# Performance work log

Measured on AMD Instinct MI355X. Metric: run time of the kernel, lower is better.

The kernel has to match this reference:

```python
import jax, jax.numpy as jnp
import numpy as np

D = 768; H = 12; DH = 64; P = 16; G = 14; NP = 196; L = 197
LD = 4; GD = 12          # local / latent depths
RL = 12; RG = 8          # tokens merged per layer (total_merge // depth)
B = 8
EPS = 1e-6


def layernorm(x, g, b):
    mu = x.mean(-1, keepdims=True)
    v = ((x - mu) ** 2).mean(-1, keepdims=True)
    return (x - mu) / jnp.sqrt(v + EPS) * g + b


def attention(x, size, qkv_w, qkv_b, pw, pb):
    # proportional attention: logits += log(token size)
    Bn, N, _ = x.shape
    qkv = (x @ qkv_w + qkv_b).reshape(Bn, N, 3, H, DH)
    q, k, v = (qkv[:, :, i].transpose(0, 2, 1, 3) for i in range(3))  # bhnd
    logits = jnp.einsum('bhqd,bhkd->bhqk', q, k) * (DH ** -0.5)
    logits = logits + jnp.log(size)[:, None, None, :, 0]
    a = jax.nn.softmax(logits, axis=-1)
    o = jnp.einsum('bhqk,bhkd->bhqd', a, v).transpose(0, 2, 1, 3).reshape(Bn, N, D)
    return o @ pw + pb, k.mean(1)  # metric = mean key over heads


def tome_merge(x, size, metric, r, tok_map):
    # ToMe bipartite soft matching + weighted-average merge + source-map update
    Bn, N, _ = x.shape
    t1, t2 = (N + 1) // 2, N // 2
    m = metric / jnp.linalg.norm(metric, axis=-1, keepdims=True)
    scores = jnp.einsum('bid,bjd->bij', m[:, ::2], m[:, 1::2])
    scores = scores.at[:, 0, :].set(-jnp.inf)  # protect cls token
    node_max, node_idx = scores.max(-1), scores.argmax(-1).astype(jnp.int32)
    order = jnp.argsort(-node_max, axis=-1).astype(jnp.int32)
    src_idx = order[:, :r]
    unm_idx = jnp.sort(order[:, r:], axis=-1)  # cls stays first
    dst_idx = jnp.take_along_axis(node_idx, src_idx, axis=1)
    bi = jnp.arange(Bn)[:, None]

    def merge_sum(v):
        a, b = v[:, ::2], v[:, 1::2]
        unm = jnp.take_along_axis(a, unm_idx[..., None], axis=1)
        s = jnp.take_along_axis(a, src_idx[..., None], axis=1)
        b = b.at[bi, dst_idx].add(s)
        return jnp.concatenate([unm, b], axis=1)

    new_size = merge_sum(size)
    new_x = merge_sum(x * size) / new_size
    # per-step old->new index map, then compose with running source map
    pos_a = jnp.zeros((Bn, t1), jnp.int32)
    pos_a = pos_a.at[bi, unm_idx].set(jnp.arange(t1 - r, dtype=jnp.int32))
    pos_a = pos_a.at[bi, src_idx].set((t1 - r) + dst_idx)
    step = jnp.zeros((Bn, N), jnp.int32)
    step = step.at[:, ::2].set(pos_a)
    step = step.at[:, 1::2].set((t1 - r) + jnp.arange(t2, dtype=jnp.int32)[None])
    return new_x, new_size, jnp.take_along_axis(step, tok_map, axis=1)


def encode(x, size, tok_map, r, p):
    ln1g, ln1b, qw, qb, pw, pb, ln2g, ln2b, f1w, f1b, f2w, f2b = p
    for i in range(ln1g.shape[0]):
        a, metric = attention(layernorm(x, ln1g[i], ln1b[i]), size, qw[i], qb[i], pw[i], pb[i])
        x = x + a
        if r > 0:
            x, size, tok_map = tome_merge(x, size, metric, r, tok_map)
        h = layernorm(x, ln2g[i], ln2b[i])
        x = x + (jax.nn.gelu(h @ f1w[i] + f1b[i], approximate=False) @ f2w[i] + f2b[i])
    return x, size, tok_map


def setup_inputs() -> dict:
    key = jax.random.key(0)
    ks = iter(jax.random.split(key, 64))
    def w(shape):
        return jax.random.normal(next(ks), shape, jnp.float32) * 0.02
    def blocks(d, pre):
        return {pre + 'ln1g': jnp.ones((d, D)), pre + 'ln1b': jnp.zeros((d, D)),
                pre + 'qkv_w': w((d, D, 3 * D)), pre + 'qkv_b': jnp.zeros((d, 3 * D)),
                pre + 'proj_w': w((d, D, D)), pre + 'proj_b': jnp.zeros((d, D)),
                pre + 'ln2g': jnp.ones((d, D)), pre + 'ln2b': jnp.zeros((d, D)),
                pre + 'fc1w': w((d, D, 4 * D)), pre + 'fc1b': jnp.zeros((d, 4 * D)),
                pre + 'fc2w': w((d, 4 * D, D)), pre + 'fc2b': jnp.zeros((d, D))}
    inp = dict(x=jax.random.normal(next(ks), (B, 3, 224, 224), jnp.float32),
               patch_w=w((3 * P * P, D)), patch_b=jnp.zeros((D,)),
               cls_tok=w((1, 1, D)), pos_emb=w((1, L, D)),
               l_ng=jnp.ones((D,)), l_nb=jnp.zeros((D,)),
               g_ng=jnp.ones((D,)), g_nb=jnp.zeros((D,)),
               head_w=w((D, 10)), head_b=jnp.zeros((10,)))
    inp.update(blocks(LD, 'l_'))
    inp.update(blocks(GD, 'g_'))
    return inp


def reference(x, patch_w, patch_b, cls_tok, pos_emb,
              l_ln1g, l_ln1b, l_qkv_w, l_qkv_b, l_proj_w, l_proj_b,
              l_ln2g, l_ln2b, l_fc1w, l_fc1b, l_fc2w, l_fc2b, l_ng, l_nb,
              g_ln1g, g_ln1b, g_qkv_w, g_qkv_b, g_proj_w, g_proj_b,
              g_ln2g, g_ln2b, g_fc1w, g_fc1b, g_fc2w, g_fc2b, g_ng, g_nb,
              head_w, head_b):
    Bn = x.shape[0]
    # non-overlapping 16x16 patchify == conv stride 16
    patches = x.reshape(Bn, 3, G, P, G, P).transpose(0, 2, 4, 1, 3, 5).reshape(Bn, NP, 3 * P * P)
    t = patches @ patch_w + patch_b
    t = jnp.concatenate([jnp.broadcast_to(cls_tok, (Bn, 1, D)), t], axis=1) + pos_emb
    size = jnp.ones((Bn, L, 1), t.dtype)
    tmap = jnp.broadcast_to(jnp.arange(L, dtype=jnp.int32)[None], (Bn, L))  # token_map_for_dtem
    lp = (l_ln1g, l_ln1b, l_qkv_w, l_qkv_b, l_proj_w, l_proj_b, l_ln2g, l_ln2b, l_fc1w, l_fc1b, l_fc2w, l_fc2b)
    xl, size, tmap = encode(t, size, tmap, RL, lp)   # local encoder: 197 -> 149 tokens
    xl = layernorm(xl, l_ng, l_nb)
    N1 = xl.shape[1]
    smap = jnp.broadcast_to(jnp.arange(N1, dtype=jnp.int32)[None], (Bn, N1))  # latent source_map
    gp = (g_ln1g, g_ln1b, g_qkv_w, g_qkv_b, g_proj_w, g_proj_b, g_ln2g, g_ln2b, g_fc1w, g_fc1b, g_fc2w, g_fc2b)
    xg, size, smap = encode(xl, size, smap, RG, gp)  # latent encoder: 149 -> 53 tokens
    xg = layernorm(xg, g_ng, g_nb)
    xr = jnp.take_along_axis(xg, smap[..., None], axis=1)   # token_unmerge_from_map (ToMe)
    xf = jnp.take_along_axis(xr, tmap[..., None], axis=1)   # token_unmerge_from_map_for_dtem
    return xf[:, 0] @ head_w + head_b  # cls token -> logits (B, 10)
```

## Files before the change

### kernel.cpp

```cpp
#include <hip/hip_runtime.h>
#include <math.h>

#define NB 8
#define SD 768
#define NHEAD 12
#define LMAX 197
#define QBLK 32
#define KBLK 64

typedef __attribute__((ext_vector_type(8))) short bf16x8;
typedef __attribute__((ext_vector_type(4))) float f32x4;
typedef const __attribute__((address_space(1))) unsigned int gu32_t;
typedef __attribute__((address_space(3))) unsigned int lu32_t;

static __device__ __forceinline__ float geluf(float x){
    return 0.5f*x*(1.0f+erff(x*0.70710678118654752440f));
}

static __device__ __forceinline__ void split_bf16(float v, ushort& h, ushort& l){
    uint u = __float_as_uint(v);
    uint hb = (u + 0x7FFFu + ((u>>16)&1u)) >> 16;
    h = (ushort)hb;
    float rem = v - __uint_as_float(hb<<16);
    uint u2 = __float_as_uint(rem);
    l = (ushort)((u2 + 0x7FFFu + ((u2>>16)&1u)) >> 16);
}

__global__ __launch_bounds__(256) void wconv(const float* __restrict__ W,
        ushort* __restrict__ Hi, ushort* __restrict__ Lo, int K, int Nc)
{
    __shared__ float tile[32][33];
    int z = blockIdx.z;
    const float* Wz = W + (size_t)z*K*Nc;
    ushort* Hz = Hi + (size_t)z*Nc*K;
    ushort* Lz = Lo + (size_t)z*Nc*K;
    int n0 = blockIdx.x*32, k0 = blockIdx.y*32;
    int tx = threadIdx.x&31, ty = threadIdx.x>>5;
    #pragma unroll
    for (int i=0;i<32;i+=8) tile[ty+i][tx] = Wz[(size_t)(k0+ty+i)*Nc + n0+tx];
    __syncthreads();
    #pragma unroll
    for (int i=0;i<32;i+=8){
        float v = tile[tx][ty+i];
        ushort h,l; split_bf16(v,h,l);
        size_t o = (size_t)(n0+ty+i)*K + k0+tx;
        Hz[o]=h; Lz[o]=l;
    }
}

template<int EPI, int SPLITK>
__global__ __launch_bounds__(256) void gemm_mfma(const ushort* __restrict__ AHi,
        const ushort* __restrict__ ALo, const ushort* __restrict__ WHi,
        const ushort* __restrict__ WLo, const float* __restrict__ bias,
        const float* __restrict__ R, float* __restrict__ C,
        ushort* __restrict__ CHi, ushort* __restrict__ CLo,
        float* __restrict__ Part, int M, int Nc, int K, int ntok, int gx)
{
    __shared__ __align__(16) ushort sAhi[2][2048], sAlo[2][2048];
    __shared__ __align__(16) ushort sBhi[2][2048], sBlo[2][2048];
    const int t = threadIdx.x;
    const int nwg = gridDim.x;
    const int qc = nwg>>3, rc = nwg&7;
    const int xcd = blockIdx.x & 7, jj = blockIdx.x >> 3;
    const int wid = (xcd<rc ? xcd*(qc+1) : rc*(qc+1)+(xcd-rc)*qc) + jj;
    const int bx = wid % gx;
    const int t2 = wid / gx;
    const int gy = nwg/(gx*SPLITK);
    const int by = t2 % gy;
    const int bz = t2 / gy;

    const int w = t>>6, l = t&63, lr = l&15, lg = l>>4;
    const int wr = w>>1, wc = w&1;

    const int Ks = K/SPLITK;
    const int kbeg = bz*Ks;
    const int nt = Ks/32;

    const int srow = t>>2;
    const uint schunk = (uint)((((t&3) ^ ((t>>3)&3)))*16);
    int ar = by*64 + srow; if (ar >= M) ar = M-1;
    int ab_ = ar/ntok; int an_ = ar - ab_*ntok;
    size_t aoff = ((size_t)(ab_*LMAX+an_)*K + kbeg)*2 + schunk;
    size_t woff = ((size_t)(bx*64+srow)*K + kbeg)*2 + schunk;
    const char* pAh = (const char*)AHi + aoff;
    const char* pAl = (const char*)ALo + aoff;
    const char* pWh = (const char*)WHi + woff;
    const char* pWl = (const char*)WLo + woff;

    f32x4 acc[2][2];
    #pragma unroll
    for (int i=0;i<2;i++)
        #pragma unroll
        for (int j=0;j<2;j++) acc[i][j] = (f32x4){0.f,0.f,0.f,0.f};

    const uint wb = (uint)(w*512);

    auto stage = [&](int bf, int kt){
        size_t ko = (size_t)kt*64;
        __builtin_amdgcn_global_load_lds((gu32_t*)(pAh+ko), (lu32_t*)&sAhi[bf][wb], 16, 0, 0);
        __builtin_amdgcn_global_load_lds((gu32_t*)(pAl+ko), (lu32_t*)&sAlo[bf][wb], 16, 0, 0);
        __builtin_amdgcn_global_load_lds((gu32_t*)(pWh+ko), (lu32_t*)&sBhi[bf][wb], 16, 0, 0);
        __builtin_amdgcn_global_load_lds((gu32_t*)(pWl+ko), (lu32_t*)&sBlo[bf][wb], 16, 0, 0);
    };

    int buf = 0;
    stage(0, 0);
    for (int kt=0; kt<nt; ++kt){
        if (kt+1 < nt){
            stage(buf^1, kt+1);
            asm volatile("s_waitcnt vmcnt(4)" ::: "memory");
        } else {
            asm volatile("s_waitcnt vmcnt(0)" ::: "memory");
        }
        __builtin_amdgcn_s_barrier();
        bf16x8 ah[2], al[2], bh[2], bl[2];
        #pragma unroll
        for (int m=0;m<2;m++){
            int row = wr*32 + m*16 + lr;
            uint off = (uint)(row*64 + ((lg ^ ((row>>1)&3))<<4));
            ah[m] = *(const bf16x8*)((const char*)&sAhi[buf][0] + off);
            al[m] = *(const bf16x8*)((const char*)&sAlo[buf][0] + off);
        }
        #pragma unroll
        for (int n=0;n<2;n++){
            int col = wc*32 + n*16 + lr;
            uint off = (uint)(col*64 + ((lg ^ ((col>>1)&3))<<4));
            bh[n] = *(const bf16x8*)((const char*)&sBhi[buf][0] + off);
            bl[n] = *(const bf16x8*)((const char*)&sBlo[buf][0] + off);
        }
        #pragma unroll
        for (int m=0;m<2;m++)
            #pragma unroll
            for (int n=0;n<2;n++){
                acc[m][n] = __builtin_amdgcn_mfma_f32_16x16x32_bf16(ah[m], bh[n], acc[m][n], 0,0,0);
                acc[m][n] = __builtin_amdgcn_mfma_f32_16x16x32_bf16(ah[m], bl[n], acc[m][n], 0,0,0);
                acc[m][n] = __builtin_amdgcn_mfma_f32_16x16x32_bf16(al[m], bh[n], acc[m][n], 0,0,0);
            }
        __builtin_amdgcn_s_barrier();
        buf ^= 1;
    }

    if (SPLITK > 1){
        float* Pz = Part + (size_t)bz*M*Nc;
        #pragma unroll
        for (int m=0;m<2;m++){
            #pragma unroll
            for (int n=0;n<2;n++){
                int gcol = bx*64 + wc*32 + n*16 + lr;
                #pragma unroll
                for (int r=0;r<4;r++){
                    int grow = by*64 + wr*32 + m*16 + lg*4 + r;
                    if (grow >= M) continue;
                    Pz[(size_t)grow*Nc + gcol] = acc[m][n][r];
                }
            }
        }
    } else {
        #pragma unroll
        for (int m=0;m<2;m++){
            #pragma unroll
            for (int n=0;n<2;n++){
                int gcol = bx*64 + wc*32 + n*16 + lr;
                float bv = bias[gcol];
                #pragma unroll
                for (int r=0;r<4;r++){
                    int grow = by*64 + wr*32 + m*16 + lg*4 + r;
                    if (grow >= M) continue;
                    int b = grow/ntok; int ni = grow - b*ntok;
                    size_t off = (size_t)(b*LMAX+ni)*Nc + gcol;
                    float v = acc[m][n][r] + bv;
                    if (EPI==1){
                        v = geluf(v);
                        ushort h,lo; split_bf16(v,h,lo);
                        CHi[off]=h; CLo[off]=lo;
                    } else {
                        if (EPI==2) v += R[off];
                        C[off] = v;
                    }
                }
            }
        }
    }
}

__global__ __launch_bounds__(256) void reduce_k(const float* __restrict__ P,
        const float* __restrict__ bias, const float* __restrict__ R,
        float* __restrict__ C, int M, int Nc, int S, int ntok)
{
    int idx = blockIdx.x*256 + threadIdx.x;
    int tot = M*(Nc/4);
    if (idx >= tot) return;
    int grow = idx/(Nc/4), c4 = idx - grow*(Nc/4);
    size_t po = (size_t)grow*Nc + c4*4;
    float4 a = *(const float4*)(P + po);
    for (int s=1;s<S;s++){
        float4 v = *(const float4*)(P + (size_t)s*M*Nc + po);
        a.x+=v.x; a.y+=v.y; a.z+=v.z; a.w+=v.w;
    }
    int b = grow/ntok, n = grow - b*ntok;
    size_t off = (size_t)(b*LMAX+n)*Nc + c4*4;
    float4 bv = *(const float4*)(bias + c4*4);
    float4 rv = *(const float4*)(R + off);
    float4 o;
    o.x=a.x+bv.x+rv.x; o.y=a.y+bv.y+rv.y; o.z=a.z+bv.z+rv.z; o.w=a.w+bv.w+rv.w;
    *(float4*)(C + off) = o;
}

__device__ __forceinline__ float block_sum256(float v){
    __shared__ float red[4];
    for (int o=32;o>0;o>>=1) v += __shfl_down(v,o,64);
    int t=threadIdx.x;
    if ((t&63)==0) red[t>>6]=v;
    __syncthreads();
    float r = red[0]+red[1]+red[2]+red[3];
    __syncthreads();
    return r;
}

__global__ __launch_bounds__(256) void ln_split(const float* __restrict__ X,
        const float* __restrict__ gam, const float* __restrict__ bet,
        ushort* __restrict__ YHi, ushort* __restrict__ YLo)
{
    int n = blockIdx.x, b = blockIdx.y, t = threadIdx.x;
    const float* xr = X + ((size_t)(b*LMAX+n))*SD;
    size_t ro = ((size_t)(b*LMAX+n))*SD;
    float v0=xr[t], v1=xr[t+256], v2=xr[t+512];
    float mu = block_sum256(v0+v1+v2) * (1.0f/768.0f);
    float d0=v0-mu, d1=v1-mu, d2=v2-mu;
    float var = block_sum256(d0*d0+d1*d1+d2*d2) * (1.0f/768.0f);
    float rs = rsqrtf(var + 1e-6f);
    float y0 = d0*rs*gam[t]     + bet[t];
    float y1 = d1*rs*gam[t+256] + bet[t+256];
    float y2 = d2*rs*gam[t+512] + bet[t+512];
    ushort h,lo;
    split_bf16(y0,h,lo); YHi[ro+t]=h;     YLo[ro+t]=lo;
    split_bf16(y1,h,lo); YHi[ro+t+256]=h; YLo[ro+t+256]=lo;
    split_bf16(y2,h,lo); YHi[ro+t+512]=h; YLo[ro+t+512]=lo;
}

__global__ __launch_bounds__(256) void ln_kernel(const float* __restrict__ X,
        const float* __restrict__ gam, const float* __restrict__ bet,
        float* __restrict__ Y)
{
    int n = blockIdx.x, b = blockIdx.y, t = threadIdx.x;
    const float* xr = X + ((size_t)(b*LMAX+n))*SD;
    float* yr = Y + ((size_t)(b*LMAX+n))*SD;
    float v0=xr[t], v1=xr[t+256], v2=xr[t+512];
    float mu = block_sum256(v0+v1+v2) * (1.0f/768.0f);
    float d0=v0-mu, d1=v1-mu, d2=v2-mu;
    float var = block_sum256(d0*d0+d1*d1+d2*d2) * (1.0f/768.0f);
    float rs = rsqrtf(var + 1e-6f);
    yr[t]     = d0*rs*gam[t]     + bet[t];
    yr[t+256] = d1*rs*gam[t+256] + bet[t+256];
    yr[t+512] = d2*rs*gam[t+512] + bet[t+512];
}

__global__ __launch_bounds__(256) void attn_tile(const float* __restrict__ QKV,
        const float* __restrict__ SZ, ushort* __restrict__ OHi,
        ushort* __restrict__ OLo, int N)
{
    const int q0 = blockIdx.x*QBLK;
    const int h = blockIdx.y, b = blockIdx.z, t = threadIdx.x;
    __shared__ float Qs[QBLK][68];
    __shared__ float KVs[KBLK][68];
    __shared__ float Ls[QBLK][200];
    __shared__ float szl[KBLK];
    __shared__ float invs[QBLK];

    {
        int row = t>>3, seg = t&7;
        int q = q0 + row;
        if (q < N){
            const float* src = QKV + ((size_t)(b*LMAX+q))*2304 + h*64 + seg*8;
            *(float4*)&Qs[row][seg*8]   = *(const float4*)src;
            *(float4*)&Qs[row][seg*8+4] = *(const float4*)(src+4);
        } else {
            float4 z = make_float4(0.f,0.f,0.f,0.f);
            *(float4*)&Qs[row][seg*8]   = z;
            *(float4*)&Qs[row][seg*8+4] = z;
        }
    }
    const int tq = t>>3, tk = t&7;
    const int nkt = (N+KBLK-1)/KBLK;

    for (int kt=0; kt<nkt; ++kt){
        int kbase = kt*KBLK;
        __syncthreads();
        {
            int row = t>>2, seg = t&3;
            int ktok = kbase + row;
            float4 a,b4,c,d4;
            if (ktok < N){
                const float* src = QKV + ((size_t)(b*LMAX+ktok))*2304 + 768 + h*64 + seg*16;
                a=*(const float4*)src; b4=*(const float4*)(src+4);
                c=*(const float4*)(src+8); d4=*(const float4*)(src+12);
            } else {
                a=b4=c=d4=make_float4(0.f,0.f,0.f,0.f);
            }
            *(float4*)&KVs[row][seg*16]   =a;
            *(float4*)&KVs[row][seg*16+4] =b4;
            *(float4*)&KVs[row][seg*16+8] =c;
            *(float4*)&KVs[row][seg*16+12]=d4;
            if (t < KBLK){
                int kk2 = kbase + t;
                szl[t] = (kk2<N) ? logf(SZ[b*LMAX+kk2]) : 0.f;
            }
        }
        __syncthreads();
        float acc[8];
        #pragma unroll
        for (int j=0;j<8;j++) acc[j]=0.f;
        #pragma unroll 4
        for (int d4=0; d4<16; ++d4){
            float4 qv = *(const float4*)&Qs[tq][d4*4];
            #pragma unroll
            for (int j=0;j<8;j++){
                float4 kv = *(const float4*)&KVs[tk+8*j][d4*4];
                acc[j] += qv.x*kv.x + qv.y*kv.y + qv.z*kv.z + qv.w*kv.w;
            }
        }
        #pragma unroll
        for (int j=0;j<8;j++){
            int kk = kbase + tk + 8*j;
            if (kk < N) Ls[tq][kk] = acc[j]*0.125f + szl[tk+8*j];
        }
    }
    __syncthreads();

    {
        float m = -INFINITY;
        for (int k=tk;k<N;k+=8) m = fmaxf(m, Ls[tq][k]);
        #pragma unroll
        for (int o=1;o<8;o<<=1) m = fmaxf(m, __shfl_xor(m,o,64));
        float s = 0.f;
        for (int k=tk;k<N;k+=8){
            float p = expf(Ls[tq][k]-m);
            Ls[tq][k]=p; s+=p;
        }
        #pragma unroll
        for (int o=1;o<8;o<<=1) s += __shfl_xor(s,o,64);
        if (tk==0) invs[tq] = 1.0f/s;
    }

    float o0[8];
    #pragma unroll
    for (int i=0;i<8;i++) o0[i]=0.f;
    for (int kt=0; kt<nkt; ++kt){
        int kbase = kt*KBLK;
        __syncthreads();
        {
            int row = t>>2, seg = t&3;
            int ktok = kbase + row;
            float4 a,b4,c,d4;
            if (ktok < N){
                const float* src = QKV + ((size_t)(b*LMAX+ktok))*2304 + 1536 + h*64 + seg*16;
                a=*(const float4*)src; b4=*(const float4*)(src+4);
                c=*(const float4*)(src+8); d4=*(const float4*)(src+12);
            } else {
                a=b4=c=d4=make_float4(0.f,0.f,0.f,0.f);
            }
            *(float4*)&KVs[row][seg*16]   =a;
            *(float4*)&KVs[row][seg*16+4] =b4;
            *(float4*)&KVs[row][seg*16+8] =c;
            *(float4*)&KVs[row][seg*16+12]=d4;
        }
        __syncthreads();
        int kmax = N - kbase; if (kmax > KBLK) kmax = KBLK;
        for (int kk=0; kk<kmax; ++kk){
            float p = Ls[tq][kbase+kk];
            float4 v0 = *(const float4*)&KVs[kk][tk*8];
            float4 v1 = *(const float4*)&KVs[kk][tk*8+4];
            o0[0]+=p*v0.x; o0[1]+=p*v0.y; o0[2]+=p*v0.z; o0[3]+=p*v0.w;
            o0[4]+=p*v1.x; o0[5]+=p*v1.y; o0[6]+=p*v1.z; o0[7]+=p*v1.w;
        }
    }
    int q = q0 + tq;
    if (q < N){
        float inv = invs[tq];
        ushort hh[8], ll[8];
        #pragma unroll
        for (int i=0;i<8;i++){ split_bf16(o0[i]*inv, hh[i], ll[i]); }
        size_t o = ((size_t)(b*LMAX+q))*SD + h*64 + tk*8;
        *(ushort4*)(OHi+o)   = make_ushort4(hh[0],hh[1],hh[2],hh[3]);
        *(ushort4*)(OHi+o+4) = make_ushort4(hh[4],hh[5],hh[6],hh[7]);
        *(ushort4*)(OLo+o)   = make_ushort4(ll[0],ll[1],ll[2],ll[3]);
        *(ushort4*)(OLo+o+4) = make_ushort4(ll[4],ll[5],ll[6],ll[7]);
    }
}

__global__ void metric_k(const float* __restrict__ QKV, float* __restrict__ MET)
{
    const int n = blockIdx.x, b = blockIdx.y, d = threadIdx.x;
    const float* base = QKV + ((size_t)(b*LMAX+n))*2304 + 768 + d;
    float s=0.f;
    #pragma unroll
    for (int h=0;h<12;h++) s += base[h*64];
    s *= (1.0f/12.0f);
    float sq = s*s;
    for (int o=32;o>0;o>>=1) sq += __shfl_down(sq,o,64);
    float nrm = sqrtf(__shfl(sq,0,64));
    MET[((size_t)(b*LMAX+n))*64 + d] = s/nrm;
}

__global__ __launch_bounds__(128) void scores_k(const float* __restrict__ MET,
        float* __restrict__ NMAX, int* __restrict__ NIDX, int t2)
{
    const int i = blockIdx.x, b = blockIdx.y, t = threadIdx.x;
    __shared__ float ma[64];
    __shared__ float vals[128];
    __shared__ int idxs[128];
    if (t<64) ma[t] = MET[((size_t)(b*LMAX+2*i))*64+t];
    __syncthreads();
    float val = -INFINITY;
    if (t<t2 && i>0){
        const float* mb = MET + ((size_t)(b*LMAX+2*t+1))*64;
        float dot=0.f;
        #pragma unroll 8
        for (int dd=0;dd<64;dd++) dot += ma[dd]*mb[dd];
        val = dot;
    }
    vals[t]=val; idxs[t]=t; __syncthreads();
    for (int s=64;s>0;s>>=1){
        if (t<s){
            float v2=vals[t+s], v1=vals[t]; int i2=idxs[t+s];
            if (v2>v1 || (v2==v1 && i2<idxs[t])){ vals[t]=v2; idxs[t]=i2; }
        }
        __syncthreads();
    }
    if (t==0){ NMAX[b*128+i]=vals[0]; NIDX[b*128+i]=idxs[0]; }
}

__global__ __launch_bounds__(128) void plan_k(const float* __restrict__ NMAX,
        const int* __restrict__ NIDX, int* __restrict__ SRC, int* __restrict__ DST,
        int* __restrict__ STEP, int* __restrict__ INV, int t1, int t2, int r)
{
    const int b = blockIdx.x, i = threadIdx.x;
    __shared__ float nm[128];
    __shared__ int issrc[128];
    nm[i] = (i<t1) ? NMAX[b*128+i] : INFINITY;
    __syncthreads();
    int rank=0, is=0, ni=0;
    if (i<t1){
        float m = nm[i];
        for (int j=0;j<t1;j++){ float a=nm[j]; if (a>m || (a==m && j<i)) rank++; }
        is = (rank<r) ? 1:0;
        ni = NIDX[b*128+i];
    }
    issrc[i]=is; __syncthreads();
    if (i<t1){
        if (is){ SRC[b*16+rank]=i; DST[b*16+rank]=ni; STEP[b*LMAX+2*i] = t1-r+ni; }
        else {
            int cnt=0;
            for (int j=0;j<i;j++) cnt += 1-issrc[j];
            STEP[b*LMAX+2*i]=cnt;
            INV[b*LMAX+cnt]=2*i;
        }
    }
    if (i<t2){ STEP[b*LMAX+2*i+1]=t1-r+i; INV[b*LMAX+(t1-r)+i]=2*i+1; }
}

__global__ __launch_bounds__(256) void merge_fused(const float* __restrict__ X,
        const float* __restrict__ SZ, const int* __restrict__ INV,
        const int* __restrict__ SRC, const int* __restrict__ DST,
        float* __restrict__ XO, float* __restrict__ SZO, int t1, int r)
{
    int p = blockIdx.x, b = blockIdx.y, t = threadIdx.x;
    int base = t1 - r;
    float acc0, acc1, acc2, snew;
    if (p < base){
        int tok = INV[b*LMAX+p];
        float s = SZ[b*LMAX+tok];
        const float* xr = X + (size_t)(b*LMAX+tok)*SD;
        acc0=xr[t]*s; acc1=xr[t+256]*s; acc2=xr[t+512]*s; snew=s;
    } else {
        int d = p - base;
        int tok = 2*d+1;
        float s = SZ[b*LMAX+tok];
        const float* xr = X + (size_t)(b*LMAX+tok)*SD;
        acc0=xr[t]*s; acc1=xr[t+256]*s; acc2=xr[t+512]*s; snew=s;
        for (int k=0;k<r;k++){
            if (DST[b*16+k]==d){
                int st = 2*SRC[b*16+k];
                float ss = SZ[b*LMAX+st];
                const float* xs = X + (size_t)(b*LMAX+st)*SD;
                acc0+=xs[t]*ss; acc1+=xs[t+256]*ss; acc2+=xs[t+512]*ss; snew+=ss;
            }
        }
    }
    float inv = 1.0f/snew;
    float* o = XO + (size_t)(b*LMAX+p)*SD;
    o[t]=acc0*inv; o[t+256]=acc1*inv; o[t+512]=acc2*inv;
    if (t==0) SZO[b*LMAX+p]=snew;
}

__global__ void map_upd(int* __restrict__ MAP, const int* __restrict__ STEP, int mlen)
{
    int i = blockIdx.x*256+threadIdx.x;
    if (i >= NB*mlen) return;
    int b=i/mlen, t=i-b*mlen;
    MAP[b*LMAX+t] = STEP[b*LMAX + MAP[b*LMAX+t]];
}

__global__ void patchify(const float* __restrict__ X, ushort* __restrict__ PHi,
        ushort* __restrict__ PLo)
{
    size_t i = (size_t)blockIdx.x*256 + threadIdx.x;
    if (i >= (size_t)NB*196*768) return;
    int f = i % 768; size_t q = i/768; int p = q % 196; int b = q/196;
    int c = f >> 8, py = (f>>4)&15, px = f&15;
    int gy = p/14, gx = p - gy*14;
    float v = X[(((size_t)b*3 + c)*224 + gy*16+py)*224 + gx*16+px];
    ushort h,l; split_bf16(v,h,l);
    size_t o = ((size_t)(b*LMAX+p))*768 + f;
    PHi[o]=h; PLo[o]=l;
}

__global__ void assemble(const float* __restrict__ T, const float* __restrict__ cls,
        const float* __restrict__ pos, float* __restrict__ Xo)
{
    size_t i = (size_t)blockIdx.x*256 + threadIdx.x;
    if (i >= (size_t)NB*LMAX*768) return;
    int d = i % 768; size_t q = i/768; int n = q % LMAX; int b = q/LMAX;
    float v = (n==0) ? cls[d] : T[((size_t)(b*LMAX+n-1))*768+d];
    Xo[((size_t)(b*LMAX+n))*768+d] = v + pos[n*768+d];
}

__global__ void init_state(float* __restrict__ SZ, int* __restrict__ TMAP, int* __restrict__ SMAP)
{
    int i = blockIdx.x*256+threadIdx.x;
    if (i >= NB*LMAX) return;
    SZ[i]=1.0f;
    int n=i%LMAX;
    TMAP[i]=n;
    if (n<149) SMAP[i]=n;
}

__global__ void head_k(const float* __restrict__ XG, const int* __restrict__ SMAP,
        const int* __restrict__ TMAP, const float* __restrict__ HW,
        const float* __restrict__ HB, float* __restrict__ OUT)
{
    int t = threadIdx.x;
    if (t>=80) return;
    int b=t/10, o=t-b*10;
    int row = SMAP[b*LMAX + TMAP[b*LMAX]];
    const float* xr = XG + ((size_t)(b*LMAX+row))*SD;
    float acc = HB[o];
    for (int d=0;d<SD;d++) acc += xr[d]*HW[d*10+o];
    OUT[b*10+o]=acc;
}

extern "C" void kernel_launch(void* const* d_in, const int* in_sizes, int n_in,
                              void* d_out, int out_size, void* d_ws, size_t ws_size,
                              hipStream_t stream)
{
    const float* x_in    = (const float*)d_in[0];
    const float* patch_w = (const float*)d_in[1];
    const float* patch_b = (const float*)d_in[2];
    const float* cls     = (const float*)d_in[3];
    const float* pos     = (const float*)d_in[4];
    const float* l_ng    = (const float*)d_in[5];
    const float* l_nb    = (const float*)d_in[6];
    const float* g_ng    = (const float*)d_in[7];
    const float* g_nb    = (const float*)d_in[8];
    const float* head_w  = (const float*)d_in[9];
    const float* head_b  = (const float*)d_in[10];
    const float* L[12];  for (int i=0;i<12;i++) L[i]  = (const float*)d_in[11+i];
    const float* Gp[12]; for (int i=0;i<12;i++) Gp[i] = (const float*)d_in[23+i];
    float* out = (float*)d_out;

    float* fp = (float*)d_ws;
    float* xA      = fp; fp += (size_t)NB*LMAX*SD;
    float* xB      = fp; fp += (size_t)NB*LMAX*SD;
    float* qkvbuf  = fp; fp += (size_t)NB*LMAX*2304;
    float* metricbuf=fp; fp += (size_t)NB*LMAX*64;
    float* partbuf = fp; fp += (size_t)4*NB*LMAX*SD;
    float* szA     = fp; fp += NB*LMAX;
    float* szB     = fp; fp += NB*LMAX;
    float* nodemax = fp; fp += NB*128;
    int* ip = (int*)fp;
    int* tmap    = ip; ip += NB*LMAX;
    int* smap    = ip; ip += NB*LMAX;
    int* stepbuf = ip; ip += NB*LMAX;
    int* invrow  = ip; ip += NB*LMAX;
    int* nodeidx = ip; ip += NB*128;
    int* srcs    = ip; ip += NB*16;
    int* dsts    = ip; ip += NB*16;
    uintptr_t up = ((uintptr_t)ip + 15) & ~(uintptr_t)15;
    ushort* sp = (ushort*)up;
    ushort* lnHi = sp; sp += (size_t)NB*LMAX*SD;
    ushort* lnLo = sp; sp += (size_t)NB*LMAX*SD;
    ushort* oHi  = sp; sp += (size_t)NB*LMAX*SD;
    ushort* oLo  = sp; sp += (size_t)NB*LMAX*SD;
    ushort* hHi  = sp; sp += (size_t)NB*LMAX*3072;
    ushort* hLo  = sp; sp += (size_t)NB*LMAX*3072;
    ushort* pHi  = sp; sp += (size_t)NB*LMAX*SD;
    ushort* pLo  = sp; sp += (size_t)NB*LMAX*SD;
    ushort* patchHi = sp; sp += (size_t)768*768;
    ushort* patchLo = sp; sp += (size_t)768*768;
    ushort* qkvHi = sp; sp += (size_t)4*768*2304;
    ushort* qkvLo = sp; sp += (size_t)4*768*2304;
    ushort* projHi= sp; sp += (size_t)4*768*768;
    ushort* projLo= sp; sp += (size_t)4*768*768;
    ushort* fc1Hi = sp; sp += (size_t)4*768*3072;
    ushort* fc1Lo = sp; sp += (size_t)4*768*3072;
    ushort* fc2Hi = sp; sp += (size_t)4*3072*768;
    ushort* fc2Lo = sp; sp += (size_t)4*3072*768;

    float *xc = xA, *xn = xB, *szc = szA, *szn = szB;

    auto conv_chunk = [&](const float* qw, const float* pw, const float* f1w,
                          const float* f2w, int nz)
    {
        wconv<<<dim3(2304/32,768/32,nz),256,0,stream>>>(qw, qkvHi, qkvLo, SD, 2304);
        wconv<<<dim3(768/32,768/32,nz),256,0,stream>>>(pw, projHi, projLo, SD, SD);
        wconv<<<dim3(3072/32,768/32,nz),256,0,stream>>>(f1w, fc1Hi, fc1Lo, SD, 3072);
        wconv<<<dim3(768/32,3072/32,nz),256,0,stream>>>(f2w, fc2Hi, fc2Lo, 3072, SD);
    };

    auto run_block = [&](const float* ln1g, const float* ln1b, const float* qb,
                         const float* pb, const float* ln2g, const float* ln2b,
                         const float* f1b, const float* f2b,
                         int slot, int N, int r, int* mp, int mlen)
    {
        int M = NB*N;
        int Mt = (M+63)/64;
        const ushort* qH = qkvHi + (size_t)slot*768*2304;
        const ushort* qL = qkvLo + (size_t)slot*768*2304;
        const ushort* pH = projHi + (size_t)slot*768*768;
        const ushort* pL = projLo + (size_t)slot*768*768;
        const ushort* f1H = fc1Hi + (size_t)slot*768*3072;
        const ushort* f1L = fc1Lo + (size_t)slot*768*3072;
        const ushort* f2H = fc2Hi + (size_t)slot*3072*768;
        const ushort* f2L = fc2Lo + (size_t)slot*3072*768;

        ln_split<<<dim3(N,NB),256,0,stream>>>(xc, ln1g, ln1b, lnHi, lnLo);
        gemm_mfma<0,1><<<36*Mt,256,0,stream>>>(lnHi, lnLo, qH, qL, qb, nullptr, qkvbuf, nullptr, nullptr, nullptr, M, 2304, SD, N, 36);
        attn_tile<<<dim3((N+QBLK-1)/QBLK,NHEAD,NB),256,0,stream>>>(qkvbuf, szc, oHi, oLo, N);
        metric_k<<<dim3(N,NB),64,0,stream>>>(qkvbuf, metricbuf);
        gemm_mfma<0,4><<<12*Mt*4,256,0,stream>>>(oHi, oLo, pH, pL, nullptr, nullptr, nullptr, nullptr, nullptr, partbuf, M, SD, SD, N, 12);
        reduce_k<<<(M*(SD/4)+255)/256,256,0,stream>>>(partbuf, pb, xc, xc, M, SD, 4, N);
        int t1=(N+1)/2, t2=N/2, Nn=N-r;
        scores_k<<<dim3(t1,NB),128,0,stream>>>(metricbuf, nodemax, nodeidx, t2);
        plan_k<<<NB,128,0,stream>>>(nodemax, nodeidx, srcs, dsts, stepbuf, invrow, t1, t2, r);
        merge_fused<<<dim3(Nn,NB),256,0,stream>>>(xc, szc, invrow, srcs, dsts, xn, szn, t1, r);
        map_upd<<<(NB*mlen+255)/256,256,0,stream>>>(mp, stepbuf, mlen);
        int M2 = NB*Nn;
        int M2t = (M2+63)/64;
        ln_split<<<dim3(Nn,NB),256,0,stream>>>(xn, ln2g, ln2b, lnHi, lnLo);
        gemm_mfma<1,1><<<48*M2t,256,0,stream>>>(lnHi, lnLo, f1H, f1L, f1b, nullptr, nullptr, hHi, hLo, nullptr, M2, 3072, SD, Nn, 48);
        gemm_mfma<0,4><<<12*M2t*4,256,0,stream>>>(hHi, hLo, f2H, f2L, nullptr, nullptr, nullptr, nullptr, nullptr, partbuf, M2, SD, 3072, Nn, 12);
        reduce_k<<<(M2*(SD/4)+255)/256,256,0,stream>>>(partbuf, f2b, xn, xn, M2, SD, 4, Nn);
        float* tf; tf=xc; xc=xn; xn=tf; tf=szc; szc=szn; szn=tf;
    };

    {
        int tot = NB*196*768;
        patchify<<<(tot+255)/256,256,0,stream>>>(x_in, pHi, pLo);
        wconv<<<dim3(768/32,768/32,1),256,0,stream>>>(patch_w, patchHi, patchLo, SD, SD);
        gemm_mfma<0,1><<<12*((NB*196+63)/64),256,0,stream>>>(pHi, pLo, patchHi, patchLo, patch_b, nullptr, qkvbuf, nullptr, nullptr, nullptr, NB*196, SD, SD, 196, 12);
        int tot2 = NB*LMAX*768;
        assemble<<<(tot2+255)/256,256,0,stream>>>(qkvbuf, cls, pos, xc);
        init_state<<<(NB*LMAX+255)/256,256,0,stream>>>(szc, tmap, smap);
    }

    conv_chunk(L[2], L[4], L[8], L[10], 4);
    int N = 197;
    for (int i=0;i<4;i++){
        run_block(L[0]+i*768, L[1]+i*768, L[3]+(size_t)i*2304,
                  L[5]+(size_t)i*768, L[6]+i*768, L[7]+i*768,
                  L[9]+(size_t)i*3072, L[11]+(size_t)i*768,
                  i, N, 12, tmap, 197);
        N -= 12;
    }
    ln_kernel<<<dim3(N,NB),256,0,stream>>>(xc, l_ng, l_nb, xc);

    for (int c=0;c<3;c++){
        conv_chunk(Gp[2]+(size_t)(4*c)*768*2304, Gp[4]+(size_t)(4*c)*768*768,
                   Gp[8]+(size_t)(4*c)*768*3072, Gp[10]+(size_t)(4*c)*3072*768, 4);
        for (int j=0;j<4;j++){
            int i = 4*c+j;
            run_block(Gp[0]+i*768, Gp[1]+i*768, Gp[3]+(size_t)i*2304,
                      Gp[5]+(size_t)i*768, Gp[6]+i*768, Gp[7]+i*768,
                      Gp[9]+(size_t)i*3072, Gp[11]+(size_t)i*768,
                      j, N, 8, smap, 149);
            N -= 8;
        }
    }
    ln_kernel<<<dim3(N,NB),256,0,stream>>>(xc, g_ng, g_nb, qkvbuf);
    head_k<<<1,128,0,stream>>>(qkvbuf, smap, tmap, head_w, head_b, out);
}
```

Measured before the change: 2.739 ms.

## Fuse map update into plan kernel, batch metric rows, add GEMM setprio

The source-map update moves into the planning kernel, which keeps the step table in shared memory. This removes one launch per layer and the global step buffer. metric_k now handles four tokens per 256-thread block instead of one per 64-thread block. The GEMM raises wave priority around its MFMA cluster and skips the trailing barrier on the last k-iteration, which adds scheduling changes whose effect is hard to predict.

```diff
diff --git a/kernel.cpp b/kernel.cpp
--- a/kernel.cpp
+++ b/kernel.cpp
@@ -128,6 +128,7 @@
             bh[n] = *(const bf16x8*)((const char*)&sBhi[buf][0] + off);
             bl[n] = *(const bf16x8*)((const char*)&sBlo[buf][0] + off);
         }
+        __builtin_amdgcn_s_setprio(1);
         #pragma unroll
         for (int m=0;m<2;m++)
             #pragma unroll
@@ -136,7 +137,8 @@
                 acc[m][n] = __builtin_amdgcn_mfma_f32_16x16x32_bf16(ah[m], bl[n], acc[m][n], 0,0,0);
                 acc[m][n] = __builtin_amdgcn_mfma_f32_16x16x32_bf16(al[m], bh[n], acc[m][n], 0,0,0);
             }
-        __builtin_amdgcn_s_barrier();
+        __builtin_amdgcn_s_setprio(0);
+        if (kt+1 < nt) __builtin_amdgcn_s_barrier();
         buf ^= 1;
     }
 
@@ -388,9 +390,13 @@
     }
 }
 
-__global__ void metric_k(const float* __restrict__ QKV, float* __restrict__ MET)
-{
-    const int n = blockIdx.x, b = blockIdx.y, d = threadIdx.x;
+__global__ __launch_bounds__(256) void metric_k(const float* __restrict__ QKV,
+        float* __restrict__ MET, int N)
+{
+    const int b = blockIdx.y;
+    const int sub = threadIdx.x>>6, d = threadIdx.x&63;
+    const int n = blockIdx.x*4 + sub;
+    if (n >= N) return;
     const float* base = QKV + ((size_t)(b*LMAX+n))*2304 + 768 + d;
     float s=0.f;
     #pragma unroll
@@ -430,13 +436,15 @@
     if (t==0){ NMAX[b*128+i]=vals[0]; NIDX[b*128+i]=idxs[0]; }
 }
 
-__global__ __launch_bounds__(128) void plan_k(const float* __restrict__ NMAX,
+__global__ __launch_bounds__(128) void plan_map(const float* __restrict__ NMAX,
         const int* __restrict__ NIDX, int* __restrict__ SRC, int* __restrict__ DST,
-        int* __restrict__ STEP, int* __restrict__ INV, int t1, int t2, int r)
+        int* __restrict__ INV, int* __restrict__ MAP,
+        int t1, int t2, int r, int mlen)
 {
     const int b = blockIdx.x, i = threadIdx.x;
     __shared__ float nm[128];
     __shared__ int issrc[128];
+    __shared__ int sstep[208];
     nm[i] = (i<t1) ? NMAX[b*128+i] : INFINITY;
     __syncthreads();
     int rank=0, is=0, ni=0;
@@ -448,15 +456,18 @@
     }
     issrc[i]=is; __syncthreads();
     if (i<t1){
-        if (is){ SRC[b*16+rank]=i; DST[b*16+rank]=ni; STEP[b*LMAX+2*i] = t1-r+ni; }
+        if (is){ SRC[b*16+rank]=i; DST[b*16+rank]=ni; sstep[2*i] = t1-r+ni; }
         else {
             int cnt=0;
             for (int j=0;j<i;j++) cnt += 1-issrc[j];
-            STEP[b*LMAX+2*i]=cnt;
+            sstep[2*i]=cnt;
             INV[b*LMAX+cnt]=2*i;
         }
     }
-    if (i<t2){ STEP[b*LMAX+2*i+1]=t1-r+i; INV[b*LMAX+(t1-r)+i]=2*i+1; }
+    if (i<t2){ sstep[2*i+1]=t1-r+i; INV[b*LMAX+(t1-r)+i]=2*i+1; }
+    __syncthreads();
+    for (int idx=i; idx<mlen; idx+=128)
+        MAP[b*LMAX+idx] = sstep[MAP[b*LMAX+idx]];
 }
 
 __global__ __launch_bounds__(256) void merge_fused(const float* __restrict__ X,
@@ -493,14 +504,6 @@
     if (t==0) SZO[b*LMAX+p]=snew;
 }
 
-__global__ void map_upd(int* __restrict__ MAP, const int* __restrict__ STEP, int mlen)
-{
-    int i = blockIdx.x*256+threadIdx.x;
-    if (i >= NB*mlen) return;
-    int b=i/mlen, t=i-b*mlen;
-    MAP[b*LMAX+t] = STEP[b*LMAX + MAP[b*LMAX+t]];
-}
-
 __global__ void patchify(const float* __restrict__ X, ushort* __restrict__ PHi,
         ushort* __restrict__ PLo)
 {
@@ -580,7 +583,6 @@
     int* ip = (int*)fp;
     int* tmap    = ip; ip += NB*LMAX;
     int* smap    = ip; ip += NB*LMAX;
-    int* stepbuf = ip; ip += NB*LMAX;
     int* invrow  = ip; ip += NB*LMAX;
     int* nodeidx = ip; ip += NB*128;
     int* srcs    = ip; ip += NB*16;
@@ -636,14 +638,13 @@
         ln_split<<<dim3(N,NB),256,0,stream>>>(xc, ln1g, ln1b, lnHi, lnLo);
         gemm_mfma<0,1><<<36*Mt,256,0,stream>>>(lnHi, lnLo, qH, qL, qb, nullptr, qkvbuf, nullptr, nullptr, nullptr, M, 2304, SD, N, 36);
         attn_tile<<<dim3((N+QBLK-1)/QBLK,NHEAD,NB),256,0,stream>>>(qkvbuf, szc, oHi, oLo, N);
-        metric_k<<<dim3(N,NB),64,0,stream>>>(qkvbuf, metricbuf);
+        metric_k<<<dim3((N+3)/4,NB),256,0,stream>>>(qkvbuf, metricbuf, N);
         gemm_mfma<0,4><<<12*Mt*4,256,0,stream>>>(oHi, oLo, pH, pL, nullptr, nullptr, nullptr, nullptr, nullptr, partbuf, M, SD, SD, N, 12);
         reduce_k<<<(M*(SD/4)+255)/256,256,0,stream>>>(partbuf, pb, xc, xc, M, SD, 4, N);
         int t1=(N+1)/2, t2=N/2, Nn=N-r;
         scores_k<<<dim3(t1,NB),128,0,stream>>>(metricbuf, nodemax, nodeidx, t2);
-        plan_k<<<NB,128,0,stream>>>(nodemax, nodeidx, srcs, dsts, stepbuf, invrow, t1, t2, r);
+        plan_map<<<NB,128,0,stream>>>(nodemax, nodeidx, srcs, dsts, invrow, mp, t1, t2, r, mlen);
         merge_fused<<<dim3(Nn,NB),256,0,stream>>>(xc, szc, invrow, srcs, dsts, xn, szn, t1, r);
-        map_upd<<<(NB*mlen+255)/256,256,0,stream>>>(mp, stepbuf, mlen);
         int M2 = NB*Nn;
         int M2t = (M2+63)/64;
         ln_split<<<dim3(Nn,NB),256,0,stream>>>(xn, ln2g, ln2b, lnHi, lnLo);
```

Measured after the change: 3.247 ms. 18.5% more time.
